# Performance work log

Hardware: AMD Instinct MI355X
Metric: run time of the kernel (lower is better)

Reference implementation:

```python
import jax, jax.numpy as jnp
import numpy as np

N_NODE, N_EDGE = 8192, 4096
D_NODE, D_EDGE, D_GLOBAL = 64, 16, 8


def _dense(key, fan_in, fan_out):
    kw, kb = jax.random.split(key)
    W = jax.random.normal(kw, (fan_in, fan_out), dtype=jnp.float32) * 0.02
    b = jnp.zeros((fan_out,), dtype=jnp.float32)
    return W, b


def setup_inputs() -> dict:
    key = jax.random.key(0)
    ks = jax.random.split(key, 16)
    nodes = jax.random.normal(ks[0], (N_NODE, D_NODE), dtype=jnp.float32)
    edges = jax.random.normal(ks[1], (N_EDGE, D_EDGE), dtype=jnp.float32)
    globals_ = jax.random.normal(ks[2], (1, D_GLOBAL), dtype=jnp.float32)
    senders = jax.random.randint(ks[3], (N_EDGE,), 0, N_NODE, dtype=jnp.int32)
    receivers = jax.random.randint(ks[4], (N_EDGE,), 0, N_NODE, dtype=jnp.int32)
    # edge MLP: input = concat(edges, nodes[s], nodes[r], globals); widths [N_EDGE]*2
    e_in = D_EDGE + 2 * D_NODE + D_GLOBAL
    eW1, eb1 = _dense(ks[5], e_in, N_EDGE)
    eW2, eb2 = _dense(ks[6], N_EDGE, N_EDGE)
    # node MLP: input = concat(nodes, sent_agg, recv_agg, globals); widths [D_NODE]*2
    n_in = D_NODE + 2 * N_EDGE + D_GLOBAL
    nW1, nb1 = _dense(ks[7], n_in, D_NODE)
    nW2, nb2 = _dense(ks[8], D_NODE, D_NODE)
    return {"nodes": nodes, "edges": edges, "globals_": globals_,
            "senders": senders, "receivers": receivers,
            "eW1": eW1, "eb1": eb1, "eW2": eW2, "eb2": eb2,
            "nW1": nW1, "nb1": nb1, "nW2": nW2, "nb2": nb2}


def reference(nodes, edges, globals_, senders, receivers,
              eW1, eb1, eW2, eb2, nW1, nb1, nW2, nb2):
    n_node, n_edge = nodes.shape[0], edges.shape[0]
    g = globals_[0]  # single graph: broadcast its global feature row
    # --- edge update: concat(edges, sent node feats, received node feats, globals) ---
    g_e = jnp.broadcast_to(g, (n_edge, g.shape[0]))
    e_in = jnp.concatenate([edges, nodes[senders], nodes[receivers], g_e], axis=-1)
    h = jax.nn.relu(e_in @ eW1 + eb1)          # [E, E]
    new_edges = jax.nn.relu(h @ eW2 + eb2)     # [E, E]
    # --- aggregate edges to nodes (jraph default: segment_sum by senders and receivers) ---
    sent_agg = jax.ops.segment_sum(new_edges, senders, num_segments=n_node)
    recv_agg = jax.ops.segment_sum(new_edges, receivers, num_segments=n_node)
    # --- node update: concat(nodes, sent_agg, recv_agg, globals) ---
    g_n = jnp.broadcast_to(g, (n_node, g.shape[0]))
    n_in = jnp.concatenate([nodes, sent_agg, recv_agg, g_n], axis=-1)
    h2 = jax.nn.relu(n_in @ nW1 + nb1)         # [N, D_NODE]
    new_nodes = jax.nn.relu(h2 @ nW2 + nb2)    # [N, D_NODE]
    # globals unchanged (update_global_fn=None)
    return new_nodes, new_edges
```

## Files before the change

kernel.cpp:

```cpp
#include <hip/hip_runtime.h>

typedef unsigned short u16;
typedef unsigned int u32;
typedef unsigned long long u64;
typedef __bf16 bf16x8 __attribute__((ext_vector_type(8)));
typedef float f32x4 __attribute__((ext_vector_type(4)));

static __device__ __forceinline__ float bf2f(u16 u) {
  return __uint_as_float(((u32)u) << 16);
}
static __device__ __forceinline__ u16 f2bf(float f) {
  u32 x = __float_as_uint(f);
  return (u16)((x + 0x7fffu + ((x >> 16) & 1u)) >> 16);
}
static __device__ __forceinline__ void gl_lds16(const u16* g, u16* l) {
  __builtin_amdgcn_global_load_lds(
      (const __attribute__((address_space(1))) void*)g,
      (__attribute__((address_space(3))) void*)l, 16, 0, 0);
}
static __device__ __forceinline__ u64 pack4bf(f32x4 v) {
  u64 r = (u64)f2bf(v[0]);
  r |= (u64)f2bf(v[1]) << 16;
  r |= (u64)f2bf(v[2]) << 32;
  r |= (u64)f2bf(v[3]) << 48;
  return r;
}

__global__ __launch_bounds__(256) void k_transpose(const float* __restrict__ in,
                                                   u16* __restrict__ out,
                                                   int K, int N, int Kpad) {
  __shared__ u16 t[64 * 68];
  const int tid = threadIdx.x;
  const int k0 = blockIdx.x * 64, n0 = blockIdx.y * 64;
#pragma unroll
  for (int pass = 0; pass < 4; pass++) {
    int ki = pass * 16 + (tid >> 4);
    int nj = (tid & 15) * 4;
    f32x4 v = {0.f, 0.f, 0.f, 0.f};
    if (k0 + ki < K) v = *(const f32x4*)&in[(long)(k0 + ki) * N + n0 + nj];
    *(u64*)&t[ki * 68 + nj] = pack4bf(v);
  }
  __syncthreads();
#pragma unroll
  for (int pass = 0; pass < 4; pass++) {
    int ni = pass * 16 + (tid >> 4);
    int kj = (tid & 15) * 4;
    if (k0 + kj < Kpad) {
      u64 w = (u64)t[(kj + 0) * 68 + ni] | ((u64)t[(kj + 1) * 68 + ni] << 16) |
              ((u64)t[(kj + 2) * 68 + ni] << 32) | ((u64)t[(kj + 3) * 68 + ni] << 48);
      *(u64*)&out[(long)(n0 + ni) * Kpad + k0 + kj] = w;
    }
  }
}

__global__ __launch_bounds__(192) void k_build_ein(const float* __restrict__ edges,
                                                   const float* __restrict__ nodes,
                                                   const float* __restrict__ g,
                                                   const int* __restrict__ senders,
                                                   const int* __restrict__ receivers,
                                                   u16* __restrict__ ein) {
  const int e = blockIdx.x;
  const int x = threadIdx.x;
  if (x >= 160) return;
  const int s = senders[e], r = receivers[e];
  float v;
  if (x < 16) v = edges[(long)e * 16 + x];
  else if (x < 80) v = nodes[(long)s * 64 + (x - 16)];
  else if (x < 144) v = nodes[(long)r * 64 + (x - 80)];
  else if (x < 152) v = g[x - 144];
  else v = 0.f;
  ein[(long)e * 160 + x] = f2bf(v);
}

template <int MODE>
__global__ __launch_bounds__(256) void k_mgemm(const u16* __restrict__ A,
                                               const u16* __restrict__ BT,
                                               const float* __restrict__ bias,
                                               void* __restrict__ C, int M, int N, int K) {
  __shared__ alignas(16) u16 As[128 * 32];
  __shared__ alignas(16) u16 Bs[128 * 32];
  const int tid = threadIdx.x;
  const int lane = tid & 63, wid = tid >> 6;
  const int wr = wid >> 1, wc = wid & 1;
  const int m0 = blockIdx.x * 128, n0 = blockIdx.y * 128;
  const int lr = lane & 15, lk = lane >> 4;
  const int swz = (lk ^ ((lr >> 1) & 3)) << 3;
  const int srow = tid >> 2;
  const int skk = ((tid & 3) ^ ((tid >> 3) & 3)) << 3;

  f32x4 acc[4][4];
#pragma unroll
  for (int i = 0; i < 4; i++)
#pragma unroll
    for (int j = 0; j < 4; j++) acc[i][j] = {0.f, 0.f, 0.f, 0.f};

  for (int kt = 0; kt < K; kt += 32) {
#pragma unroll
    for (int rep = 0; rep < 2; rep++) {
      int row = rep * 64 + srow;
      int o = rep * 2048 + tid * 8;
      gl_lds16(&A[(long)(m0 + row) * K + kt + skk], &As[o]);
      gl_lds16(&BT[(long)(n0 + row) * K + kt + skk], &Bs[o]);
    }
    __syncthreads();
    bf16x8 af[4], bfr[4];
#pragma unroll
    for (int mi = 0; mi < 4; mi++)
      af[mi] = *(const bf16x8*)&As[(wr * 64 + mi * 16 + lr) * 32 + swz];
#pragma unroll
    for (int ni = 0; ni < 4; ni++)
      bfr[ni] = *(const bf16x8*)&Bs[(wc * 64 + ni * 16 + lr) * 32 + swz];
#pragma unroll
    for (int mi = 0; mi < 4; mi++)
#pragma unroll
      for (int ni = 0; ni < 4; ni++)
        acc[mi][ni] =
            __builtin_amdgcn_mfma_f32_16x16x32_bf16(af[mi], bfr[ni], acc[mi][ni], 0, 0, 0);
    __syncthreads();
  }
#pragma unroll
  for (int ni = 0; ni < 4; ni++) {
    int col = n0 + wc * 64 + ni * 16 + lr;
    float bb = bias[col];
#pragma unroll
    for (int mi = 0; mi < 4; mi++) {
      int row = m0 + wr * 64 + mi * 16 + lk * 4;
#pragma unroll
      for (int r = 0; r < 4; r++) {
        float v = fmaxf(acc[mi][ni][r] + bb, 0.f);
        if (MODE == 0) ((u16*)C)[(long)(row + r) * N + col] = f2bf(v);
        else ((float*)C)[(long)(row + r) * N + col] = v;
      }
    }
  }
}

__global__ __launch_bounds__(512, 1) void k_gemm256(const u16* __restrict__ A,
                                                    const u16* __restrict__ BT,
                                                    const float* __restrict__ bias,
                                                    float* __restrict__ C, int N, int K) {
  __shared__ alignas(16) u16 lds[65536];
  const int tid = threadIdx.x;
  const int lane = tid & 63, wid = tid >> 6;
  const int wr = wid >> 2, wc = wid & 3;
  const int orig = blockIdx.x;
  const int xc = orig & 7, jj = orig >> 3;
  const int m0 = (2 * xc + (jj >> 4)) * 256;
  const int n0 = (jj & 15) * 256;
  const int lr = lane & 15, lk = lane >> 4;
  const int swz = (lk ^ ((lr >> 1) & 3)) << 3;
  const int NT = K >> 5;

  const int srow = wid * 16 + (lane >> 2);
  const int sq = ((lane & 3) ^ ((lane >> 3) & 3)) << 3;
  const int sdst = wid * 512 + lane * 8;

  f32x4 acc[8][4];
#pragma unroll
  for (int i = 0; i < 8; i++)
#pragma unroll
    for (int j = 0; j < 4; j++) acc[i][j] = {0.f, 0.f, 0.f, 0.f};

#define STAGE_TILE(T)                                                              \
  {                                                                                \
    const int kt_ = (T) * 32;                                                      \
    u16* Ab_ = &lds[((T) & 3) * 16384];                                            \
    u16* Bb_ = Ab_ + 8192;                                                         \
    gl_lds16(&A[(long)(m0 + srow) * K + kt_ + sq], Ab_ + sdst);                    \
    gl_lds16(&A[(long)(m0 + 128 + srow) * K + kt_ + sq], Ab_ + 4096 + sdst);       \
    gl_lds16(&BT[(long)(n0 + srow) * K + kt_ + sq], Bb_ + sdst);                   \
    gl_lds16(&BT[(long)(n0 + 128 + srow) * K + kt_ + sq], Bb_ + 4096 + sdst);      \
  }

  STAGE_TILE(0)
  STAGE_TILE(1)
  STAGE_TILE(2)

  for (int t = 0; t < NT; t++) {
    if (t < NT - 2) {
      asm volatile("s_waitcnt vmcnt(8)" ::: "memory");
    } else if (t == NT - 2) {
      asm volatile("s_waitcnt vmcnt(4)" ::: "memory");
    } else {
      asm volatile("s_waitcnt vmcnt(0)" ::: "memory");
    }
    __builtin_amdgcn_s_barrier();
    if (t + 3 < NT) STAGE_TILE(t + 3)

    const u16* Ab = &lds[(t & 3) * 16384];
    const u16* Bb = Ab + 8192;
    bf16x8 af[8], bfr[4];
#pragma unroll
    for (int mi = 0; mi < 8; mi++)
      af[mi] = *(const bf16x8*)&Ab[(wr * 128 + mi * 16 + lr) * 32 + swz];
#pragma unroll
    for (int ni = 0; ni < 4; ni++)
      bfr[ni] = *(const bf16x8*)&Bb[(wc * 64 + ni * 16 + lr) * 32 + swz];
#pragma unroll
    for (int mi = 0; mi < 8; mi++)
#pragma unroll
      for (int ni = 0; ni < 4; ni++)
        acc[mi][ni] =
            __builtin_amdgcn_mfma_f32_16x16x32_bf16(af[mi], bfr[ni], acc[mi][ni], 0, 0, 0);
  }
#undef STAGE_TILE

#pragma unroll
  for (int ni = 0; ni < 4; ni++) {
    int col = n0 + wc * 64 + ni * 16 + lr;
    float bb = bias[col];
#pragma unroll
    for (int mi = 0; mi < 8; mi++) {
      int row = m0 + wr * 128 + mi * 16 + lk * 4;
#pragma unroll
      for (int r = 0; r < 4; r++)
        C[(long)(row + r) * N + col] = fmaxf(acc[mi][ni][r] + bb, 0.f);
    }
  }
}

__global__ __launch_bounds__(256) void k_scatter_m(const float* __restrict__ E,
                                                   const u16* __restrict__ BT,
                                                   const int* __restrict__ senders,
                                                   const int* __restrict__ receivers,
                                                   float* __restrict__ accb) {
  const int K = 4096;
  __shared__ alignas(16) u16 As[128 * 32];
  __shared__ alignas(16) u16 Bs[128 * 32];
  const int tid = threadIdx.x;
  const int lane = tid & 63, wid = tid >> 6;
  const int wr = wid >> 1, wc = wid & 1;
  const int m0 = blockIdx.x * 128;
  const int kbase = blockIdx.y * 512;
  const int lr = lane & 15, lk = lane >> 4;
  const int swz = (lk ^ ((lr >> 1) & 3)) << 3;
  const int srow = tid >> 2;
  const int skk = ((tid & 3) ^ ((tid >> 3) & 3)) << 3;

  f32x4 acc[4][4];
#pragma unroll
  for (int i = 0; i < 4; i++)
#pragma unroll
    for (int j = 0; j < 4; j++) acc[i][j] = {0.f, 0.f, 0.f, 0.f};

  for (int kt = kbase; kt < kbase + 512; kt += 32) {
#pragma unroll
    for (int p = 0; p < 4; p++) {
      int idx = p * 256 + tid;
      int r = idx >> 3;
      int kq = idx & 7;
      f32x4 v = *(const f32x4*)&E[(long)(m0 + r) * 4096 + kt + kq * 4];
      int gq = (kq >> 1) ^ ((r >> 1) & 3);
      *(u64*)&As[r * 32 + gq * 8 + (kq & 1) * 4] = pack4bf(v);
    }
#pragma unroll
    for (int rep = 0; rep < 2; rep++) {
      int row = rep * 64 + srow;
      gl_lds16(&BT[(long)row * K + kt + skk], &Bs[rep * 2048 + tid * 8]);
    }
    __syncthreads();
    bf16x8 af[4], bfr[4];
#pragma unroll
    for (int mi = 0; mi < 4; mi++)
      af[mi] = *(const bf16x8*)&As[(wr * 64 + mi * 16 + lr) * 32 + swz];
#pragma unroll
    for (int ni = 0; ni < 4; ni++)
      bfr[ni] = *(const bf16x8*)&Bs[(wc * 64 + ni * 16 + lr) * 32 + swz];
#pragma unroll
    for (int mi = 0; mi < 4; mi++)
#pragma unroll
      for (int ni = 0; ni < 4; ni++)
        acc[mi][ni] =
            __builtin_amdgcn_mfma_f32_16x16x32_bf16(af[mi], bfr[ni], acc[mi][ni], 0, 0, 0);
    __syncthreads();
  }
#pragma unroll
  for (int mi = 0; mi < 4; mi++) {
#pragma unroll
    for (int r = 0; r < 4; r++) {
      int e = m0 + wr * 64 + mi * 16 + lk * 4 + r;
#pragma unroll
      for (int ni = 0; ni < 4; ni++) {
        int col = wc * 64 + ni * 16 + lr;
        int tgt = (col < 64) ? senders[e] : receivers[e];
        atomicAdd(&accb[(long)tgt * 64 + (col & 63)], acc[mi][ni][r]);
      }
    }
  }
}

__global__ __launch_bounds__(256) void k_final(const float* __restrict__ nodes,
                                               const float* __restrict__ g,
                                               const float* __restrict__ nW1,
                                               const float* __restrict__ nb1,
                                               const float* __restrict__ nW2,
                                               const float* __restrict__ nb2,
                                               const float* __restrict__ zpre,
                                               float* __restrict__ out0) {
  __shared__ float h2[64 * 64];
  __shared__ float gb[64];
  const int tid = threadIdx.x;
  const long n0 = (long)blockIdx.x * 64;
  if (tid < 64) {
    float s = nb1[tid];
#pragma unroll
    for (int j = 0; j < 8; j++) s += g[j] * nW1[(long)(8256 + j) * 64 + tid];
    gb[tid] = s;
  }
  __syncthreads();
#pragma unroll 2
  for (int rep = 0; rep < 16; rep++) {
    int idx = rep * 256 + tid;
    int i = idx >> 6, c = idx & 63;
    float z = gb[c] + zpre[(n0 + i) * 64 + c];
    const float* nr = nodes + (n0 + i) * 64;
#pragma unroll 8
    for (int k = 0; k < 64; k++) z += nr[k] * nW1[(long)k * 64 + c];
    h2[idx] = fmaxf(z, 0.f);
  }
  __syncthreads();
#pragma unroll 2
  for (int rep = 0; rep < 16; rep++) {
    int idx = rep * 256 + tid;
    int i = idx >> 6, c = idx & 63;
    float z = nb2[c];
#pragma unroll 8
    for (int k = 0; k < 64; k++) z += h2[i * 64 + k] * nW2[(long)k * 64 + c];
    out0[(n0 + i) * 64 + c] = fmaxf(z, 0.f);
  }
}

extern "C" void kernel_launch(void* const* d_in, const int* in_sizes, int n_in,
                              void* d_out, int out_size, void* d_ws, size_t ws_size,
                              hipStream_t stream) {
  const float* nodes = (const float*)d_in[0];
  const float* edges = (const float*)d_in[1];
  const float* g = (const float*)d_in[2];
  const int* senders = (const int*)d_in[3];
  const int* receivers = (const int*)d_in[4];
  const float* eW1 = (const float*)d_in[5];
  const float* eb1 = (const float*)d_in[6];
  const float* eW2 = (const float*)d_in[7];
  const float* eb2 = (const float*)d_in[8];
  const float* nW1 = (const float*)d_in[9];
  const float* nb1 = (const float*)d_in[10];
  const float* nW2 = (const float*)d_in[11];
  const float* nb2 = (const float*)d_in[12];

  char* ws = (char*)d_ws;
  u16* eW1T = (u16*)(ws + 0);
  float* accb = (float*)(ws + 0);
  u16* ein = (u16*)(ws + 2097152);
  u16* nWmT = (u16*)(ws + 2097152);
  u16* eW2T = (u16*)(ws + 3407872);
  u16* h = (u16*)(ws + 36962304);

  float* out_nodes = (float*)d_out;
  float* out_edges = (float*)d_out + 524288;

  dim3 b256(256);
  k_transpose<<<dim3(3, 64), b256, 0, stream>>>(eW1, eW1T, 152, 4096, 160);
  k_transpose<<<dim3(64, 64), b256, 0, stream>>>(eW2, eW2T, 4096, 4096, 4096);
  k_build_ein<<<4096, 192, 0, stream>>>(edges, nodes, g, senders, receivers, ein);

  k_mgemm<0><<<dim3(32, 32), b256, 0, stream>>>(ein, eW1T, eb1, h, 4096, 4096, 160);

  k_transpose<<<dim3(64, 1), b256, 0, stream>>>(nW1 + 64 * 64, nWmT, 4096, 64, 4096);
  k_transpose<<<dim3(64, 1), b256, 0, stream>>>(nW1 + 4160 * 64, nWmT + (long)64 * 4096,
                                                4096, 64, 4096);
  hipMemsetAsync(accb, 0, 8192 * 64 * 4, stream);

  k_gemm256<<<dim3(256), dim3(512), 0, stream>>>(h, eW2T, eb2, out_edges, 4096, 4096);

  k_scatter_m<<<dim3(32, 8), b256, 0, stream>>>(out_edges, nWmT, senders, receivers, accb);
  k_final<<<128, b256, 0, stream>>>(nodes, g, nW1, nb1, nW2, nb2, accb, out_nodes);
}
```

Before: 252.4 us.

## Restructure GEMM main loop to 64-wide K tiles with double buffering

The 256x256 bf16 GEMM now stages 64-element K tiles into two LDS buffers instead of 32-element tiles in a four-deep ring. This halves the number of loop iterations and barriers per K, and it uses an 8-granule XOR swizzle for the wider rows. Each tile is consumed in two MFMA phases with an explicit lgkmcnt wait, a sched_barrier and raised wave priority around the MFMA bursts. The trade-off is a shallower prefetch depth and an extra barrier before restaging, which could expose more global-load latency.

```diff
diff --git a/kernel.cpp b/kernel.cpp
--- a/kernel.cpp
+++ b/kernel.cpp
@@ -148,12 +148,12 @@
   const int m0 = (2 * xc + (jj >> 4)) * 256;
   const int n0 = (jj & 15) * 256;
   const int lr = lane & 15, lk = lane >> 4;
-  const int swz = (lk ^ ((lr >> 1) & 3)) << 3;
-  const int NT = K >> 5;
-
-  const int srow = wid * 16 + (lane >> 2);
-  const int sq = ((lane & 3) ^ ((lane >> 3) & 3)) << 3;
-  const int sdst = wid * 512 + lane * 8;
+  const int NT = K >> 6;
+
+  const int sgran = ((tid & 7) ^ ((tid >> 3) & 7)) << 3;
+  const int sdst = tid * 8;
+  const long abase = (long)(m0 + (tid >> 3)) * K + sgran;
+  const long bbase = (long)(n0 + (tid >> 3)) * K + sgran;
 
   f32x4 acc[8][4];
 #pragma unroll
@@ -161,49 +161,61 @@
 #pragma unroll
     for (int j = 0; j < 4; j++) acc[i][j] = {0.f, 0.f, 0.f, 0.f};
 
-#define STAGE_TILE(T)                                                              \
+#define STAGE64(T, BUF)                                     \
+  {                                                         \
+    const long ko_ = (long)(T) * 64;                        \
+    u16* Ab_ = &lds[(BUF) * 32768];                         \
+    u16* Bb_ = Ab_ + 16384;                                 \
+    gl_lds16(&A[abase + ko_], Ab_ + sdst);                  \
+    gl_lds16(&A[abase + (long)64 * K + ko_], Ab_ + 4096 + sdst);   \
+    gl_lds16(&A[abase + (long)128 * K + ko_], Ab_ + 8192 + sdst);  \
+    gl_lds16(&A[abase + (long)192 * K + ko_], Ab_ + 12288 + sdst); \
+    gl_lds16(&BT[bbase + ko_], Bb_ + sdst);                 \
+    gl_lds16(&BT[bbase + (long)64 * K + ko_], Bb_ + 4096 + sdst);  \
+    gl_lds16(&BT[bbase + (long)128 * K + ko_], Bb_ + 8192 + sdst); \
+    gl_lds16(&BT[bbase + (long)192 * K + ko_], Bb_ + 12288 + sdst);\
+  }
+
+#define RSWZ(R, G) (((R) * 64) + ((((G) ^ ((R) & 7))) << 3))
+
+#define PHASE(KS, AbP, BbP)                                                        \
   {                                                                                \
-    const int kt_ = (T) * 32;                                                      \
-    u16* Ab_ = &lds[((T) & 3) * 16384];                                            \
-    u16* Bb_ = Ab_ + 8192;                                                         \
-    gl_lds16(&A[(long)(m0 + srow) * K + kt_ + sq], Ab_ + sdst);                    \
-    gl_lds16(&A[(long)(m0 + 128 + srow) * K + kt_ + sq], Ab_ + 4096 + sdst);       \
-    gl_lds16(&BT[(long)(n0 + srow) * K + kt_ + sq], Bb_ + sdst);                   \
-    gl_lds16(&BT[(long)(n0 + 128 + srow) * K + kt_ + sq], Bb_ + 4096 + sdst);      \
-  }
-
-  STAGE_TILE(0)
-  STAGE_TILE(1)
-  STAGE_TILE(2)
+    bf16x8 af[8], bfr[4];                                                          \
+    _Pragma("unroll") for (int mi = 0; mi < 8; mi++)                               \
+        af[mi] = *(const bf16x8*)&AbP[RSWZ(wr * 128 + mi * 16 + lr, lk + 4 * (KS))]; \
+    _Pragma("unroll") for (int ni = 0; ni < 4; ni++)                               \
+        bfr[ni] = *(const bf16x8*)&BbP[RSWZ(wc * 64 + ni * 16 + lr, lk + 4 * (KS))]; \
+    asm volatile("s_waitcnt lgkmcnt(0)" ::: "memory");                             \
+    __builtin_amdgcn_sched_barrier(0);                                             \
+    __builtin_amdgcn_s_setprio(1);                                                 \
+    _Pragma("unroll") for (int mi = 0; mi < 8; mi++)                               \
+        _Pragma("unroll") for (int ni = 0; ni < 4; ni++)                           \
+            acc[mi][ni] = __builtin_amdgcn_mfma_f32_16x16x32_bf16(af[mi], bfr[ni], \
+                                                                  acc[mi][ni],    \
+                                                                  0, 0, 0);        \
+    __builtin_amdgcn_s_setprio(0);                                                 \
+  }
+
+  STAGE64(0, 0)
+  STAGE64(1, 1)
 
   for (int t = 0; t < NT; t++) {
-    if (t < NT - 2) {
+    if (t == NT - 1) {
+      asm volatile("s_waitcnt vmcnt(0)" ::: "memory");
+    } else {
       asm volatile("s_waitcnt vmcnt(8)" ::: "memory");
-    } else if (t == NT - 2) {
-      asm volatile("s_waitcnt vmcnt(4)" ::: "memory");
-    } else {
-      asm volatile("s_waitcnt vmcnt(0)" ::: "memory");
     }
     __builtin_amdgcn_s_barrier();
-    if (t + 3 < NT) STAGE_TILE(t + 3)
-
-    const u16* Ab = &lds[(t & 3) * 16384];
-    const u16* Bb = Ab + 8192;
-    bf16x8 af[8], bfr[4];
-#pragma unroll
-    for (int mi = 0; mi < 8; mi++)
-      af[mi] = *(const bf16x8*)&Ab[(wr * 128 + mi * 16 + lr) * 32 + swz];
-#pragma unroll
-    for (int ni = 0; ni < 4; ni++)
-      bfr[ni] = *(const bf16x8*)&Bb[(wc * 64 + ni * 16 + lr) * 32 + swz];
-#pragma unroll
-    for (int mi = 0; mi < 8; mi++)
-#pragma unroll
-      for (int ni = 0; ni < 4; ni++)
-        acc[mi][ni] =
-            __builtin_amdgcn_mfma_f32_16x16x32_bf16(af[mi], bfr[ni], acc[mi][ni], 0, 0, 0);
-  }
-#undef STAGE_TILE
+    const u16* Ab = &lds[(t & 1) * 32768];
+    const u16* Bb = Ab + 16384;
+    PHASE(0, Ab, Bb)
+    PHASE(1, Ab, Bb)
+    __builtin_amdgcn_s_barrier();
+    if (t + 2 < NT) STAGE64(t + 2, t & 1)
+  }
+#undef PHASE
+#undef RSWZ
+#undef STAGE64
 
 #pragma unroll
   for (int ni = 0; ni < 4; ni++) {
```

Result: no change. 251.1 us (-0.5%).

## Split GEMM K-loop into two half-phases interleaving A/B staging with MFMA

Applied to the files above, without the earlier changes.

Restructures the 256x256 GEMM main loop into two phases per K-tile. Each phase loads half of the A fragments, issues half of the global-to-LDS prefetch for a later tile, and runs its MFMAs under raised wave priority (s_setprio), with barriers and lgkmcnt waits separating the phases. The aim is to spread memory issue between compute bursts and keep the matrix units busy, in the style of a ping-pong schedule. The cost is more barriers per iteration and a more fragile vmcnt accounting for the 4-buffer ring.

```diff
diff --git a/kernel.cpp b/kernel.cpp
--- a/kernel.cpp
+++ b/kernel.cpp
@@ -161,49 +161,76 @@
 #pragma unroll
     for (int j = 0; j < 4; j++) acc[i][j] = {0.f, 0.f, 0.f, 0.f};
 
-#define STAGE_TILE(T)                                                              \
-  {                                                                                \
-    const int kt_ = (T) * 32;                                                      \
-    u16* Ab_ = &lds[((T) & 3) * 16384];                                            \
-    u16* Bb_ = Ab_ + 8192;                                                         \
-    gl_lds16(&A[(long)(m0 + srow) * K + kt_ + sq], Ab_ + sdst);                    \
-    gl_lds16(&A[(long)(m0 + 128 + srow) * K + kt_ + sq], Ab_ + 4096 + sdst);       \
-    gl_lds16(&BT[(long)(n0 + srow) * K + kt_ + sq], Bb_ + sdst);                   \
-    gl_lds16(&BT[(long)(n0 + 128 + srow) * K + kt_ + sq], Bb_ + 4096 + sdst);      \
-  }
-
-  STAGE_TILE(0)
-  STAGE_TILE(1)
-  STAGE_TILE(2)
+#define STAGE_A(T)                                                         \
+  {                                                                        \
+    const int kt_ = (T) * 32;                                              \
+    u16* Ab_ = &lds[((T) & 3) * 16384];                                    \
+    gl_lds16(&A[(long)(m0 + srow) * K + kt_ + sq], Ab_ + sdst);            \
+    gl_lds16(&A[(long)(m0 + 128 + srow) * K + kt_ + sq], Ab_ + 4096 + sdst);\
+  }
+#define STAGE_B(T)                                                         \
+  {                                                                        \
+    const int kt_ = (T) * 32;                                              \
+    u16* Bb_ = &lds[((T) & 3) * 16384] + 8192;                             \
+    gl_lds16(&BT[(long)(n0 + srow) * K + kt_ + sq], Bb_ + sdst);           \
+    gl_lds16(&BT[(long)(n0 + 128 + srow) * K + kt_ + sq], Bb_ + 4096 + sdst);\
+  }
+
+  STAGE_A(0) STAGE_B(0)
+  STAGE_A(1) STAGE_B(1)
+  STAGE_A(2) STAGE_B(2)
+  asm volatile("s_waitcnt vmcnt(8)" ::: "memory");
+  __builtin_amdgcn_s_barrier();
 
   for (int t = 0; t < NT; t++) {
-    if (t < NT - 2) {
-      asm volatile("s_waitcnt vmcnt(8)" ::: "memory");
-    } else if (t == NT - 2) {
-      asm volatile("s_waitcnt vmcnt(4)" ::: "memory");
-    } else {
-      asm volatile("s_waitcnt vmcnt(0)" ::: "memory");
-    }
-    __builtin_amdgcn_s_barrier();
-    if (t + 3 < NT) STAGE_TILE(t + 3)
-
     const u16* Ab = &lds[(t & 3) * 16384];
     const u16* Bb = Ab + 8192;
-    bf16x8 af[8], bfr[4];
-#pragma unroll
-    for (int mi = 0; mi < 8; mi++)
-      af[mi] = *(const bf16x8*)&Ab[(wr * 128 + mi * 16 + lr) * 32 + swz];
+    bf16x8 afA[4], afB[4], bf[4];
+#pragma unroll
+    for (int mi = 0; mi < 4; mi++)
+      afA[mi] = *(const bf16x8*)&Ab[(wr * 128 + mi * 16 + lr) * 32 + swz];
 #pragma unroll
     for (int ni = 0; ni < 4; ni++)
-      bfr[ni] = *(const bf16x8*)&Bb[(wc * 64 + ni * 16 + lr) * 32 + swz];
-#pragma unroll
-    for (int mi = 0; mi < 8; mi++)
+      bf[ni] = *(const bf16x8*)&Bb[(wc * 64 + ni * 16 + lr) * 32 + swz];
+    if (t + 3 < NT) STAGE_A(t + 3)
+    __builtin_amdgcn_s_barrier();
+    asm volatile("s_waitcnt lgkmcnt(0)" ::: "memory");
+    __builtin_amdgcn_sched_barrier(0);
+    __builtin_amdgcn_s_setprio(1);
+#pragma unroll
+    for (int mi = 0; mi < 4; mi++)
 #pragma unroll
       for (int ni = 0; ni < 4; ni++)
         acc[mi][ni] =
-            __builtin_amdgcn_mfma_f32_16x16x32_bf16(af[mi], bfr[ni], acc[mi][ni], 0, 0, 0);
-  }
-#undef STAGE_TILE
+            __builtin_amdgcn_mfma_f32_16x16x32_bf16(afA[mi], bf[ni], acc[mi][ni], 0, 0, 0);
+    __builtin_amdgcn_s_setprio(0);
+    __builtin_amdgcn_s_barrier();
+#pragma unroll
+    for (int mi = 0; mi < 4; mi++)
+      afB[mi] = *(const bf16x8*)&Ab[(wr * 128 + 64 + mi * 16 + lr) * 32 + swz];
+    if (t + 3 < NT) STAGE_B(t + 3)
+    __builtin_amdgcn_s_barrier();
+    asm volatile("s_waitcnt lgkmcnt(0)" ::: "memory");
+    __builtin_amdgcn_sched_barrier(0);
+    __builtin_amdgcn_s_setprio(1);
+#pragma unroll
+    for (int mi = 0; mi < 4; mi++)
+#pragma unroll
+      for (int ni = 0; ni < 4; ni++)
+        acc[4 + mi][ni] =
+            __builtin_amdgcn_mfma_f32_16x16x32_bf16(afB[mi], bf[ni], acc[4 + mi][ni], 0, 0, 0);
+    __builtin_amdgcn_s_setprio(0);
+    if (t < NT - 3) {
+      asm volatile("s_waitcnt vmcnt(8)" ::: "memory");
+    } else if (t == NT - 3) {
+      asm volatile("s_waitcnt vmcnt(4)" ::: "memory");
+    } else if (t == NT - 2) {
+      asm volatile("s_waitcnt vmcnt(0)" ::: "memory");
+    }
+    __builtin_amdgcn_s_barrier();
+  }
+#undef STAGE_B
+#undef STAGE_A
 
 #pragma unroll
   for (int ni = 0; ni < 4; ni++) {
```

After: 255.9 us, median of 4. About the same (+1.4%).
